# Kernel optimization log

Measured on AMD Instinct MI355X. Metric: run time of the kernel, lower is better.

Reference implementation:

```python
import jax, jax.numpy as jnp
import numpy as np
from jax import lax

THRESHOLDS = (0.25, 0.5, 0.75)
TAU = 100.0
NUM_CLASSES = 10
K = 32
RES_Z = 5.0
# each of the 16 binary logic gates is bilinear: g(a,b) = c0 + c1*a + c2*b + c3*a*b
GATE_COEF = jnp.array([
    [0, 0, 0, 0],   # 0: False
    [0, 0, 0, 1],   # 1: a AND b
    [0, 1, 0, -1],  # 2: a AND NOT b
    [0, 1, 0, 0],   # 3: a  (residual gate)
    [0, 0, 1, -1],  # 4: NOT a AND b
    [0, 0, 1, 0],   # 5: b
    [0, 1, 1, -2],  # 6: XOR
    [0, 1, 1, -1],  # 7: OR
    [1, -1, -1, 1], # 8: NOR
    [1, -1, -1, 2], # 9: XNOR
    [1, 0, -1, 0],  # 10: NOT b
    [1, 0, -1, 1],  # 11: a OR NOT b
    [1, -1, 0, 0],  # 12: NOT a
    [1, -1, 0, 1],  # 13: NOT a OR b
    [1, 0, 0, -1],  # 14: NAND
    [1, 0, 0, 0],   # 15: True
], dtype=jnp.float32)


def _gate_logits(key, shape):
    # residual init: pass-through gate (id 3) dominates
    w = 0.01 * jax.random.normal(key, shape, dtype=jnp.float32)
    return w.at[..., 3].add(RES_Z)


def _leaf_idx(rng, C, O, leaves=8, cpt=2, kk=9):
    # each tree uses cpt random input channels; each leaf picks one of them and a 3x3 position
    ch2 = rng.integers(0, C, size=(O, cpt))
    sel = rng.integers(0, cpt, size=(O, leaves))
    ch = np.take_along_axis(ch2, sel, axis=1)
    pos = rng.integers(0, kk, size=(O, leaves))
    return jnp.asarray(ch * kk + pos, dtype=jnp.int32)


def setup_inputs() -> dict:
    key = jax.random.key(0)
    ks = jax.random.split(key, 9)
    rng = np.random.default_rng(0)
    B = 128
    d = {"x": jax.random.uniform(ks[0], (B, 3, 32, 32), dtype=jnp.float32)}
    in_chs = [3 * len(THRESHOLDS), K, 4 * K, 16 * K]
    out_chs = [K, 4 * K, 16 * K, 32 * K]
    for i, (ci, co) in enumerate(zip(in_chs, out_chs)):
        d[f"c{i+1}_idx"] = _leaf_idx(rng, ci, co)
        d[f"c{i+1}_w"] = _gate_logits(ks[1 + i], (co, 7, 16))
    dims = [32 * K * 4, 1280 * K, 640 * K, 320 * K]
    for i in range(3):
        di, do = dims[i], dims[i + 1]
        d[f"l{i+1}_a"] = jnp.asarray(rng.integers(0, di, size=(do,)), dtype=jnp.int32)
        d[f"l{i+1}_b"] = jnp.asarray(rng.integers(0, di, size=(do,)), dtype=jnp.int32)
        d[f"l{i+1}_w"] = _gate_logits(ks[5 + i], (do, 16))
    return d


def _mix(logits):
    # softmax over 16 gates folded into 4 bilinear coefficients (fused gate mixture)
    return jax.nn.softmax(logits, axis=-1) @ GATE_COEF


def binarize(x):
    return jnp.concatenate([(x > t).astype(x.dtype) for t in THRESHOLDS], axis=1)


def tree_conv(x, leaf_idx, logits):
    # x: (B,C,H,W); leaf_idx: (O,8) into C*9 channel-major patch; logits: (O,7,16)
    B, C, H, W = x.shape
    xp = jnp.pad(x, ((0, 0), (0, 0), (1, 1), (1, 1)))
    patches = jnp.stack([xp[:, :, i:i + H, j:j + W] for i in range(3) for j in range(3)], axis=2)
    patches = patches.reshape(B, C * 9, H, W)
    vals = patches[:, leaf_idx]  # (B,O,8,H,W)
    m = _mix(logits)             # (O,7,4)
    node = 0
    for lvl in (4, 2, 1):
        a, b = vals[:, :, 0::2], vals[:, :, 1::2]
        w = m[:, node:node + lvl]  # (O,lvl,4)
        w0 = w[..., 0][None, :, :, None, None]
        w1 = w[..., 1][None, :, :, None, None]
        w2 = w[..., 2][None, :, :, None, None]
        w3 = w[..., 3][None, :, :, None, None]
        vals = w0 + w1 * a + w2 * b + w3 * (a * b)
        node += lvl
    return vals[:, :, 0]  # (B,O,H,W)


def or_pool(x):
    # OR of relaxed binary values == max pool 2x2/2
    return lax.reduce_window(x, -jnp.inf, lax.max, (1, 1, 2, 2), (1, 1, 2, 2), "VALID")


def logic_layer(x, a_idx, b_idx, logits):
    a = x[:, a_idx]  # (B,O)
    b = x[:, b_idx]
    w = _mix(logits)  # (O,4)
    return w[:, 0] + w[:, 1] * a + w[:, 2] * b + w[:, 3] * (a * b)


def group_sum(x):
    B = x.shape[0]
    return x.reshape(B, NUM_CLASSES, -1).sum(axis=-1) / TAU


def reference(x, c1_idx, c1_w, c2_idx, c2_w, c3_idx, c3_w, c4_idx, c4_w,
              l1_a, l1_b, l1_w, l2_a, l2_b, l2_w, l3_a, l3_b, l3_w):
    h = binarize(x)
    h = or_pool(tree_conv(h, c1_idx, c1_w))
    h = or_pool(tree_conv(h, c2_idx, c2_w))
    h = or_pool(tree_conv(h, c3_idx, c3_w))
    h = or_pool(tree_conv(h, c4_idx, c4_w))
    h = h.reshape(h.shape[0], -1)  # (B, 4096)
    h = logic_layer(h, l1_a, l1_b, l1_w)
    h = logic_layer(h, l2_a, l2_b, l2_w)
    h = logic_layer(h, l3_a, l3_b, l3_w)
    return group_sum(h)  # (B, 10)
```

## Files before the change

kernel.cpp:

```cpp
#include <hip/hip_runtime.h>
#include <hip/hip_fp16.h>

typedef float v2f __attribute__((ext_vector_type(2)));
typedef float v4f __attribute__((ext_vector_type(4)));
typedef int   v4i __attribute__((ext_vector_type(4)));

__device__ __constant__ float GC[16][4] = {
  {0,0,0,0},{0,0,0,1},{0,1,0,-1},{0,1,0,0},
  {0,0,1,-1},{0,0,1,0},{0,1,1,-2},{0,1,1,-1},
  {1,-1,-1,1},{1,-1,-1,2},{1,0,-1,0},{1,0,-1,1},
  {1,-1,0,0},{1,-1,0,1},{1,0,0,-1},{1,0,0,0}};

__device__ __forceinline__ v2f pk_mul(v2f a, v2f b) {
  v2f d;
  asm("v_pk_mul_f32 %0, %1, %2" : "=v"(d) : "v"(a), "v"(b));
  return d;
}
__device__ __forceinline__ v2f gate2pk(v2f a, v2f b, v2f w01, v2f w23) {
  v2f t = pk_mul(a, b);
  v2f d;
  asm("v_pk_fma_f32 %0, %1, %2, %2 op_sel:[0,1,0] op_sel_hi:[1,1,0]"
      : "=v"(d) : "v"(a), "v"(w01));
  asm("v_pk_fma_f32 %0, %1, %2, %0 op_sel:[0,0,0] op_sel_hi:[1,0,1]"
      : "+v"(d) : "v"(b), "v"(w23));
  asm("v_pk_fma_f32 %0, %1, %2, %0 op_sel:[0,1,0] op_sel_hi:[1,1,1]"
      : "+v"(d) : "v"(t), "v"(w23));
  return d;
}

__device__ __forceinline__ void mix_one(const float* lp, float* op) {
  float e[16];
  float s = 0.f;
  #pragma unroll
  for (int i = 0; i < 16; ++i) { e[i] = __expf(lp[i]); s += e[i]; }
  float inv = 1.0f / s;
  float w0 = 0.f, w1 = 0.f, w2 = 0.f, w3 = 0.f;
  #pragma unroll
  for (int i = 0; i < 16; ++i) {
    float p = e[i] * inv;
    w0 = fmaf(p, GC[i][0], w0);
    w1 = fmaf(p, GC[i][1], w1);
    w2 = fmaf(p, GC[i][2], w2);
    w3 = fmaf(p, GC[i][3], w3);
  }
  op[0] = w0; op[1] = w1; op[2] = w2; op[3] = w3;
}

struct PrepArgs {
  const float* logits[7];
  float* outm[7];
  const int* cidx[4];
  int* offt[4];
};

__global__ __launch_bounds__(256) void prep_k(PrepArgs A) {
  int gid = blockIdx.x * 256 + threadIdx.x;
  if (gid < 83552) {
    const int n[7] = {224, 896, 3584, 7168, 40960, 20480, 10240};
    int g = gid, seg = 0;
    while (seg < 6 && g >= n[seg]) { g -= n[seg]; ++seg; }
    mix_one(A.logits[seg] + (size_t)g * 16, A.outm[seg] + (size_t)g * 4);
  } else if (gid < 85248) {
    int r = gid - 83552;
    int L, rr;
    if (r < 32)       { L = 0; rr = r;       }
    else if (r < 160) { L = 1; rr = r - 32;  }
    else if (r < 672) { L = 2; rr = r - 160; }
    else              { L = 3; rr = r - 672; }
    const int W2Pt[4] = {35, 19, 12, 6};
    const int CSt[4]  = {1190, 342, 120, 37};
    const int swzt[4] = {1, 1, 1, 0};
    int W2P = W2Pt[L], CS = CSt[L], swz = swzt[L];
    const int* ci = A.cidx[L] + rr * 8;
    int* oo = A.offt[L] + rr * 8;
    #pragma unroll
    for (int l = 0; l < 8; ++l) {
      int idx = ci[l];
      int c  = idx / 9;
      int k  = idx - 9 * c;
      int di = k / 3 - 1;
      int dj = k - 3 * (k / 3) - 1;
      int yl = 1 + di;
      int off = c * CS + yl * W2P + 1 + dj;
      if (swz)
        off |= (((yl >> 1) & 1) << 28) | ((((yl + 1) >> 1) & 1) << 29);
      oo[l] = off;
    }
  }
}

struct MegaArgs {
  const float* x;
  const float* mc[4];
  const int*   offt[4];
  const int*   la[3];
  const int*   lb[3];
  const float* mlw[3];
  float* out;
};

extern __shared__ char S[];

template<int OH, int OW, int LOGOW, int IW2P, int PIXCNT, int LOGPIX,
         int NCH, int ITERS, bool UNI, bool RSWZ, bool OHALO, int OW2P,
         int OCS, bool OSWZ>
__device__ __forceinline__ void conv_stage(
    const float* in, float* outb,
    const int* __restrict__ offt, const float* __restrict__ mtab, int tid) {
  int pix = tid & (PIXCNT - 1);
  int ch0 = tid >> LOGPIX;
  int pw  = pix & (OW - 1);
  int ph  = pix >> LOGOW;
  int pixbase = 2 * ph * IW2P + 2 * pw;
  int ph1 = ph & 1;
  #pragma unroll 4
  for (int it = 0; it < ITERS; ++it) {
    int ch = ch0 + NCH * it;
    if (UNI) ch = __builtin_amdgcn_readfirstlane(ch);
    const int* ot = offt + ch * 8;
    const float* mt = mtab + ch * 28;
    v4f g0 = *(const v4f*)(mt +  0);
    v4f g1 = *(const v4f*)(mt +  4);
    v4f g2 = *(const v4f*)(mt +  8);
    v4f g3 = *(const v4f*)(mt + 12);
    v4f g4 = *(const v4f*)(mt + 16);
    v4f g5 = *(const v4f*)(mt + 20);
    v4f g6 = *(const v4f*)(mt + 24);
    v2f v01[8], v23[8];
    #pragma unroll
    for (int l = 0; l < 8; ++l) {
      int e = ot[l];
      int at, ab;
      if (RSWZ) {
        int off = e & 0x0FFFFFFF;
        at = off + pixbase + ((ph1 ^ (e >> 28)) & 1);
        ab = off + pixbase + IW2P + ((ph1 ^ (e >> 29)) & 1);
      } else {
        at = e + pixbase;
        ab = at + IW2P;
      }
      v2f t0; t0.x = in[at]; t0.y = in[at + 1];
      v2f t1; t1.x = in[ab]; t1.y = in[ab + 1];
      v01[l] = t0; v23[l] = t1;
    }
    v2f u0 = gate2pk(v01[0], v01[1], g0.xy, g0.zw);
    v2f u1 = gate2pk(v01[2], v01[3], g1.xy, g1.zw);
    v2f u2 = gate2pk(v01[4], v01[5], g2.xy, g2.zw);
    v2f u3 = gate2pk(v01[6], v01[7], g3.xy, g3.zw);
    v2f s0 = gate2pk(u0, u1, g4.xy, g4.zw);
    v2f s1 = gate2pk(u2, u3, g5.xy, g5.zw);
    v2f r0 = gate2pk(s0, s1, g6.xy, g6.zw);
    u0 = gate2pk(v23[0], v23[1], g0.xy, g0.zw);
    u1 = gate2pk(v23[2], v23[3], g1.xy, g1.zw);
    u2 = gate2pk(v23[4], v23[5], g2.xy, g2.zw);
    u3 = gate2pk(v23[6], v23[7], g3.xy, g3.zw);
    s0 = gate2pk(u0, u1, g4.xy, g4.zw);
    s1 = gate2pk(u2, u3, g5.xy, g5.zw);
    v2f r1 = gate2pk(s0, s1, g6.xy, g6.zw);
    float res = fmaxf(fmaxf(r0.x, r0.y), fmaxf(r1.x, r1.y));
    if (OHALO) {
      int oy = 1 + ph;
      int widx = ch * OCS + oy * OW2P + 1 + pw;
      if (OSWZ) widx += (oy >> 1) & 1;
      outb[widx] = res;
    } else {
      outb[ch * (OH * OW) + pix] = res;
    }
  }
}

__global__ __launch_bounds__(1024) void mega_k(MegaArgs A) {
  int tid = threadIdx.x;
  int b = blockIdx.x;
  float* binb = (float*)(S);
  float* buf1 = (float*)(S + 61440);
  float* buf2 = (float*)(S);
  float* buf3 = (float*)(S + 61440);
  float* h4   = (float*)(S);
  __half* g1h = (__half*)(S + 16384);
  __half* g2h = (__half*)(S + 98304);
  float* lsum = (float*)(S + 139264);
  const v4f z4 = {0.f, 0.f, 0.f, 0.f};

  for (int i = 4 * tid; i < 10712; i += 4096) *(v4f*)(binb + i) = z4;
  if (tid < 10) lsum[tid] = 0.f;
  __syncthreads();
  const float* xb = A.x + (size_t)b * 3072;
  #pragma unroll
  for (int i = 0; i < 3; ++i) {
    int idx = tid + 1024 * i;
    float v = xb[idx];
    int rgb = idx >> 10;
    int rem = idx & 1023;
    int y = rem >> 5, xx = rem & 31;
    int oy = 1 + y;
    int base = oy * 35 + 1 + xx + ((oy >> 1) & 1);
    binb[(0 + rgb) * 1190 + base] = v > 0.25f ? 1.f : 0.f;
    binb[(3 + rgb) * 1190 + base] = v > 0.50f ? 1.f : 0.f;
    binb[(6 + rgb) * 1190 + base] = v > 0.75f ? 1.f : 0.f;
  }
  __syncthreads();

  for (int i = 4 * tid; i < 10944; i += 4096) *(v4f*)(buf1 + i) = z4;
  __syncthreads();
  conv_stage<16,16,4, 35, 256,8, 4, 8, true, true, true, 19, 342, true>(
      binb, buf1, A.offt[0], A.mc[0], tid);
  __syncthreads();
  for (int i = 4 * tid; i < 15360; i += 4096) *(v4f*)(buf2 + i) = z4;
  __syncthreads();
  conv_stage<8,8,3, 19, 64,6, 16, 8, true, true, true, 12, 120, true>(
      buf1, buf2, A.offt[1], A.mc[1], tid);
  __syncthreads();
  for (int i = 4 * tid; i < 18944; i += 4096) *(v4f*)(buf3 + i) = z4;
  __syncthreads();
  conv_stage<4,4,2, 12, 16,4, 64, 8, false, true, true, 6, 37, false>(
      buf2, buf3, A.offt[2], A.mc[2], tid);
  __syncthreads();
  conv_stage<2,2,1, 6, 4,2, 256, 4, false, false, false, 1, 4, false>(
      buf3, h4, A.offt[3], A.mc[3], tid);
  __syncthreads();

  {
    const v4i* a4 = (const v4i*)A.la[0];
    const v4i* b4 = (const v4i*)A.lb[0];
    const v4f* w4 = (const v4f*)A.mlw[0];
    #pragma unroll 2
    for (int g = 0; g < 10; ++g) {
      int q = tid + 1024 * g;
      v4i ai = a4[q], bi = b4[q];
      float r[4];
      #pragma unroll
      for (int i = 0; i < 4; ++i) {
        v4f w = w4[4 * q + i];
        float a = h4[ai[i]], bb = h4[bi[i]];
        r[i] = fmaf(w.w, a * bb, fmaf(w.z, bb, fmaf(w.y, a, w.x)));
      }
      union { __half2 h[2]; uint2 u; } P;
      P.h[0] = __floats2half2_rn(r[0], r[1]);
      P.h[1] = __floats2half2_rn(r[2], r[3]);
      *(uint2*)(g1h + 4 * q) = P.u;
    }
  }
  __syncthreads();
  {
    const v4i* a4 = (const v4i*)A.la[1];
    const v4i* b4 = (const v4i*)A.lb[1];
    const v4f* w4 = (const v4f*)A.mlw[1];
    #pragma unroll 2
    for (int g = 0; g < 5; ++g) {
      int q = tid + 1024 * g;
      v4i ai = a4[q], bi = b4[q];
      float r[4];
      #pragma unroll
      for (int i = 0; i < 4; ++i) {
        v4f w = w4[4 * q + i];
        float a = __half2float(g1h[ai[i]]), bb = __half2float(g1h[bi[i]]);
        r[i] = fmaf(w.w, a * bb, fmaf(w.z, bb, fmaf(w.y, a, w.x)));
      }
      union { __half2 h[2]; uint2 u; } P;
      P.h[0] = __floats2half2_rn(r[0], r[1]);
      P.h[1] = __floats2half2_rn(r[2], r[3]);
      *(uint2*)(g2h + 4 * q) = P.u;
    }
  }
  __syncthreads();
  {
    const v4i* a4 = (const v4i*)A.la[2];
    const v4i* b4 = (const v4i*)A.lb[2];
    const v4f* w4 = (const v4f*)A.mlw[2];
    int lane = tid & 63;
    #pragma unroll
    for (int g = 0; g < 3; ++g) {
      int q = tid + 1024 * g;
      if (q < 2560) {
        v4i ai = a4[q], bi = b4[q];
        float s = 0.f;
        #pragma unroll
        for (int i = 0; i < 4; ++i) {
          v4f w = w4[4 * q + i];
          float a = __half2float(g2h[ai[i]]), bb = __half2float(g2h[bi[i]]);
          s += fmaf(w.w, a * bb, fmaf(w.z, bb, fmaf(w.y, a, w.x)));
        }
        #pragma unroll
        for (int m = 1; m < 64; m <<= 1) s += __shfl_xor(s, m);
        if (lane == 0) atomicAdd(&lsum[q >> 8], s);
      }
    }
  }
  __syncthreads();
  if (tid < 10) A.out[b * 10 + tid] = lsum[tid] * 0.01f;
}

extern "C" void kernel_launch(void* const* d_in, const int* in_sizes, int n_in,
                              void* d_out, int out_size, void* d_ws, size_t ws_size,
                              hipStream_t stream) {
  const float* x   = (const float*)d_in[0];
  const int*   c1i = (const int*)d_in[1];
  const float* c1w = (const float*)d_in[2];
  const int*   c2i = (const int*)d_in[3];
  const float* c2w = (const float*)d_in[4];
  const int*   c3i = (const int*)d_in[5];
  const float* c3w = (const float*)d_in[6];
  const int*   c4i = (const int*)d_in[7];
  const float* c4w = (const float*)d_in[8];
  const int*   l1a = (const int*)d_in[9];
  const int*   l1b = (const int*)d_in[10];
  const float* l1w = (const float*)d_in[11];
  const int*   l2a = (const int*)d_in[12];
  const int*   l2b = (const int*)d_in[13];
  const float* l2w = (const float*)d_in[14];
  const int*   l3a = (const int*)d_in[15];
  const int*   l3b = (const int*)d_in[16];
  const float* l3w = (const float*)d_in[17];

  float* ws = (float*)d_ws;
  float* mc1 = ws;
  float* mc2 = mc1 + 896;
  float* mc3 = mc2 + 3584;
  float* mc4 = mc3 + 14336;
  float* ml1 = mc4 + 28672;
  float* ml2 = ml1 + 163840;
  float* ml3 = ml2 + 81920;
  int* off1 = (int*)(ml3 + 40960);
  int* off2 = off1 + 256;
  int* off3 = off2 + 1024;
  int* off4 = off3 + 4096;

  PrepArgs P;
  P.logits[0] = c1w; P.outm[0] = mc1;
  P.logits[1] = c2w; P.outm[1] = mc2;
  P.logits[2] = c3w; P.outm[2] = mc3;
  P.logits[3] = c4w; P.outm[3] = mc4;
  P.logits[4] = l1w; P.outm[4] = ml1;
  P.logits[5] = l2w; P.outm[5] = ml2;
  P.logits[6] = l3w; P.outm[6] = ml3;
  P.cidx[0] = c1i; P.offt[0] = off1;
  P.cidx[1] = c2i; P.offt[1] = off2;
  P.cidx[2] = c3i; P.offt[2] = off3;
  P.cidx[3] = c4i; P.offt[3] = off4;
  prep_k<<<333, 256, 0, stream>>>(P);

  MegaArgs M;
  M.x = x;
  M.mc[0] = mc1; M.mc[1] = mc2; M.mc[2] = mc3; M.mc[3] = mc4;
  M.offt[0] = off1; M.offt[1] = off2; M.offt[2] = off3; M.offt[3] = off4;
  M.la[0] = l1a; M.lb[0] = l1b; M.mlw[0] = ml1;
  M.la[1] = l2a; M.lb[1] = l2b; M.mlw[1] = ml2;
  M.la[2] = l3a; M.lb[2] = l3b; M.mlw[2] = ml3;
  M.out = (float*)d_out;

  static bool attr_set = false;
  if (!attr_set) {
    hipFuncSetAttribute((const void*)mega_k,
                        hipFuncAttributeMaxDynamicSharedMemorySize, 139328);
    attr_set = true;
  }
  mega_k<<<128, 1024, 139328, stream>>>(M);
}
```

Baseline: 155.5 us.

## Split each sample across two blocks with global-memory halo exchange

Launches two blocks per sample instead of one, each computing half the rows of every conv stage and half the outputs of every logic layer. After each stage the blocks exchange boundary rows or layer halves through a global workspace, synchronised by per-sample atomic flags with release/acquire spin-waits. The aim is to use 256 CUs on the MI355X rather than 128. The cost is extra global traffic, many cross-block barriers, and a deadlock risk if the two blocks of a pair are not co-resident, since both must be running at the same time for the spin-waits to complete.

```diff
diff --git a/kernel.cpp b/kernel.cpp
--- a/kernel.cpp
+++ b/kernel.cpp
@@ -51,6 +51,7 @@
   float* outm[7];
   const int* cidx[4];
   int* offt[4];
+  int* flags;
 };
 
 __global__ __launch_bounds__(256) void prep_k(PrepArgs A) {
@@ -68,7 +69,7 @@
     else if (r < 672) { L = 2; rr = r - 160; }
     else              { L = 3; rr = r - 672; }
     const int W2Pt[4] = {35, 19, 12, 6};
-    const int CSt[4]  = {1190, 342, 120, 37};
+    const int CSt[4]  = {1190, 342, 121, 37};
     const int swzt[4] = {1, 1, 1, 0};
     int W2P = W2Pt[L], CS = CSt[L], swz = swzt[L];
     const int* ci = A.cidx[L] + rr * 8;
@@ -86,6 +87,8 @@
         off |= (((yl >> 1) & 1) << 28) | ((((yl + 1) >> 1) & 1) << 29);
       oo[l] = off;
     }
+  } else if (gid < 86272) {
+    A.flags[gid - 85248] = 0;
   }
 }
 
@@ -96,21 +99,24 @@
   const int*   la[3];
   const int*   lb[3];
   const float* mlw[3];
+  int*   flags;
+  float* ex;
   float* out;
 };
 
 extern __shared__ char S[];
 
-template<int OH, int OW, int LOGOW, int IW2P, int PIXCNT, int LOGPIX,
+template<int OWF, int LOGOW, int IW2P, int PIXH, int LOGPIXH,
          int NCH, int ITERS, bool UNI, bool RSWZ, bool OHALO, int OW2P,
-         int OCS, bool OSWZ>
+         int OCS, bool OSWZ, int OHW>
 __device__ __forceinline__ void conv_stage(
     const float* in, float* outb,
-    const int* __restrict__ offt, const float* __restrict__ mtab, int tid) {
-  int pix = tid & (PIXCNT - 1);
-  int ch0 = tid >> LOGPIX;
-  int pw  = pix & (OW - 1);
-  int ph  = pix >> LOGOW;
+    const int* __restrict__ offt, const float* __restrict__ mtab,
+    int tid, int ph0) {
+  int pix = tid & (PIXH - 1);
+  int ch0 = tid >> LOGPIXH;
+  int pw  = pix & (OWF - 1);
+  int ph  = (pix >> LOGOW) + ph0;
   int pixbase = 2 * ph * IW2P + 2 * pw;
   int ph1 = ph & 1;
   #pragma unroll 4
@@ -164,23 +170,44 @@
       if (OSWZ) widx += (oy >> 1) & 1;
       outb[widx] = res;
     } else {
-      outb[ch * (OH * OW) + pix] = res;
-    }
-  }
+      outb[ch * OHW + ph * OWF + pw] = res;
+    }
+  }
+}
+
+__device__ __forceinline__ void sigf(int* f) {
+  if (threadIdx.x == 0)
+    __hip_atomic_fetch_add(f, 1, __ATOMIC_RELEASE, __HIP_MEMORY_SCOPE_AGENT);
+}
+__device__ __forceinline__ void waitf(int* f, int v) {
+  if (threadIdx.x == 0)
+    while (__hip_atomic_load(f, __ATOMIC_ACQUIRE, __HIP_MEMORY_SCOPE_AGENT) < v)
+      __builtin_amdgcn_s_sleep(8);
 }
 
 __global__ __launch_bounds__(1024) void mega_k(MegaArgs A) {
   int tid = threadIdx.x;
-  int b = blockIdx.x;
+  int b = blockIdx.x & 127;
+  int h = blockIdx.x >> 7;
+  int hp = 1 - h;
   float* binb = (float*)(S);
-  float* buf1 = (float*)(S + 61440);
+  float* buf1 = (float*)(S + 61952);
   float* buf2 = (float*)(S);
-  float* buf3 = (float*)(S + 61440);
+  float* buf3 = (float*)(S + 61952);
   float* h4   = (float*)(S);
   __half* g1h = (__half*)(S + 16384);
   __half* g2h = (__half*)(S + 98304);
   float* lsum = (float*)(S + 139264);
   const v4f z4 = {0.f, 0.f, 0.f, 0.f};
+
+  int*   flg = A.flags + b * 8;
+  float* exb = A.ex + (size_t)b * 46080;
+  float* e1g  = exb;
+  float* e2g  = exb + 1216;
+  float* e3g  = exb + 4288;
+  float* e4g  = exb + 10432;
+  float* eg1g = exb + 14528;
+  float* eg2g = exb + 35008;
 
   for (int i = 4 * tid; i < 10712; i += 4096) *(v4f*)(binb + i) = z4;
   if (tid < 10) lsum[tid] = 0.f;
@@ -203,21 +230,82 @@
 
   for (int i = 4 * tid; i < 10944; i += 4096) *(v4f*)(buf1 + i) = z4;
   __syncthreads();
-  conv_stage<16,16,4, 35, 256,8, 4, 8, true, true, true, 19, 342, true>(
-      binb, buf1, A.offt[0], A.mc[0], tid);
-  __syncthreads();
-  for (int i = 4 * tid; i < 15360; i += 4096) *(v4f*)(buf2 + i) = z4;
-  __syncthreads();
-  conv_stage<8,8,3, 19, 64,6, 16, 8, true, true, true, 12, 120, true>(
-      buf1, buf2, A.offt[1], A.mc[1], tid);
+  conv_stage<16,4,35,128,7, 8,4, true, true, true,19,342,true, 256>(
+      binb, buf1, A.offt[0], A.mc[0], tid, 8 * h);
+  __syncthreads();
+  for (int i = 4 * tid; i < 15488; i += 4096) *(v4f*)(buf2 + i) = z4;
+  if (tid < 608) {
+    int c = tid / 19, x = tid - c * 19;
+    e1g[h * 608 + tid] = buf1[c * 342 + (8 + h) * 19 + x];
+  }
+  __threadfence();
+  __syncthreads();
+  sigf(flg + 0);
+  waitf(flg + 0, 2);
+  __syncthreads();
+  if (tid < 608) {
+    int c = tid / 19, x = tid - c * 19;
+    buf1[c * 342 + (9 - h) * 19 + x] = e1g[hp * 608 + tid];
+  }
+  __syncthreads();
+
+  conv_stage<8,3,19,32,5, 32,4, false, true, true,12,121,true, 64>(
+      buf1, buf2, A.offt[1], A.mc[1], tid, 4 * h);
   __syncthreads();
   for (int i = 4 * tid; i < 18944; i += 4096) *(v4f*)(buf3 + i) = z4;
-  __syncthreads();
-  conv_stage<4,4,2, 12, 16,4, 64, 8, false, true, true, 6, 37, false>(
-      buf2, buf3, A.offt[2], A.mc[2], tid);
-  __syncthreads();
-  conv_stage<2,2,1, 6, 4,2, 256, 4, false, false, false, 1, 4, false>(
-      buf3, h4, A.offt[3], A.mc[3], tid);
+  for (int i = tid; i < 1536; i += 1024) {
+    int c = i / 12, x = i - c * 12;
+    e2g[h * 1536 + i] = buf2[c * 121 + (4 + h) * 12 + x];
+  }
+  __threadfence();
+  __syncthreads();
+  sigf(flg + 1);
+  waitf(flg + 1, 2);
+  __syncthreads();
+  for (int i = tid; i < 1536; i += 1024) {
+    int c = i / 12, x = i - c * 12;
+    buf2[c * 121 + (5 - h) * 12 + x] = e2g[hp * 1536 + i];
+  }
+  __syncthreads();
+
+  conv_stage<4,2,12,8,3, 128,4, false, true, true,6,37,false, 16>(
+      buf2, buf3, A.offt[2], A.mc[2], tid, 2 * h);
+  __syncthreads();
+  for (int i = tid; i < 3072; i += 1024) {
+    int c = i / 6, x = i - c * 6;
+    e3g[h * 3072 + i] = buf3[c * 37 + (2 + h) * 6 + x];
+  }
+  __threadfence();
+  __syncthreads();
+  sigf(flg + 2);
+  waitf(flg + 2, 2);
+  __syncthreads();
+  for (int i = tid; i < 3072; i += 1024) {
+    int c = i / 6, x = i - c * 6;
+    buf3[c * 37 + (3 - h) * 6 + x] = e3g[hp * 3072 + i];
+  }
+  __syncthreads();
+
+  conv_stage<2,1,6,2,1, 512,2, false, false, false,1,4,false, 4>(
+      buf3, h4, A.offt[3], A.mc[3], tid, h);
+  __syncthreads();
+  #pragma unroll
+  for (int g = 0; g < 2; ++g) {
+    int t2 = tid + 1024 * g;
+    int c = t2 >> 1, j = t2 & 1;
+    e4g[h * 2048 + t2] = h4[c * 4 + 2 * h + j];
+  }
+  __threadfence();
+  __syncthreads();
+  sigf(flg + 3);
+  waitf(flg + 3, 2);
+  __syncthreads();
+  #pragma unroll
+  for (int g = 0; g < 2; ++g) {
+    int t2 = tid + 1024 * g;
+    int c = t2 >> 1, j = t2 & 1;
+    h4[c * 4 + 2 * hp + j] = e4g[hp * 2048 + t2];
+  }
   __syncthreads();
 
   {
@@ -225,8 +313,8 @@
     const v4i* b4 = (const v4i*)A.lb[0];
     const v4f* w4 = (const v4f*)A.mlw[0];
     #pragma unroll 2
-    for (int g = 0; g < 10; ++g) {
-      int q = tid + 1024 * g;
+    for (int g = 0; g < 5; ++g) {
+      int q = h * 5120 + tid + 1024 * g;
       v4i ai = a4[q], bi = b4[q];
       float r[4];
       #pragma unroll
@@ -235,44 +323,76 @@
         float a = h4[ai[i]], bb = h4[bi[i]];
         r[i] = fmaf(w.w, a * bb, fmaf(w.z, bb, fmaf(w.y, a, w.x)));
       }
-      union { __half2 h[2]; uint2 u; } P;
-      P.h[0] = __floats2half2_rn(r[0], r[1]);
-      P.h[1] = __floats2half2_rn(r[2], r[3]);
+      union { __half2 hh[2]; uint2 u; } P;
+      P.hh[0] = __floats2half2_rn(r[0], r[1]);
+      P.hh[1] = __floats2half2_rn(r[2], r[3]);
       *(uint2*)(g1h + 4 * q) = P.u;
     }
   }
   __syncthreads();
+  {
+    float* g1f = (float*)g1h;
+    #pragma unroll
+    for (int g = 0; g < 10; ++g) { int i = tid + 1024 * g; eg1g[h * 10240 + i] = g1f[h * 10240 + i]; }
+    __threadfence();
+    __syncthreads();
+    sigf(flg + 4);
+    waitf(flg + 4, 2);
+    __syncthreads();
+    #pragma unroll
+    for (int g = 0; g < 10; ++g) { int i = tid + 1024 * g; g1f[hp * 10240 + i] = eg1g[hp * 10240 + i]; }
+  }
+  __syncthreads();
+
   {
     const v4i* a4 = (const v4i*)A.la[1];
     const v4i* b4 = (const v4i*)A.lb[1];
     const v4f* w4 = (const v4f*)A.mlw[1];
     #pragma unroll 2
-    for (int g = 0; g < 5; ++g) {
-      int q = tid + 1024 * g;
-      v4i ai = a4[q], bi = b4[q];
-      float r[4];
-      #pragma unroll
-      for (int i = 0; i < 4; ++i) {
-        v4f w = w4[4 * q + i];
-        float a = __half2float(g1h[ai[i]]), bb = __half2float(g1h[bi[i]]);
-        r[i] = fmaf(w.w, a * bb, fmaf(w.z, bb, fmaf(w.y, a, w.x)));
+    for (int g = 0; g < 3; ++g) {
+      int qr = tid + 1024 * g;
+      if (qr < 2560) {
+        int q = h * 2560 + qr;
+        v4i ai = a4[q], bi = b4[q];
+        float r[4];
+        #pragma unroll
+        for (int i = 0; i < 4; ++i) {
+          v4f w = w4[4 * q + i];
+          float a = __half2float(g1h[ai[i]]), bb = __half2float(g1h[bi[i]]);
+          r[i] = fmaf(w.w, a * bb, fmaf(w.z, bb, fmaf(w.y, a, w.x)));
+        }
+        union { __half2 hh[2]; uint2 u; } P;
+        P.hh[0] = __floats2half2_rn(r[0], r[1]);
+        P.hh[1] = __floats2half2_rn(r[2], r[3]);
+        *(uint2*)(g2h + 4 * q) = P.u;
       }
-      union { __half2 h[2]; uint2 u; } P;
-      P.h[0] = __floats2half2_rn(r[0], r[1]);
-      P.h[1] = __floats2half2_rn(r[2], r[3]);
-      *(uint2*)(g2h + 4 * q) = P.u;
-    }
-  }
-  __syncthreads();
+    }
+  }
+  __syncthreads();
+  {
+    float* g2f = (float*)g2h;
+    #pragma unroll
+    for (int g = 0; g < 5; ++g) { int i = tid + 1024 * g; eg2g[h * 5120 + i] = g2f[h * 5120 + i]; }
+    __threadfence();
+    __syncthreads();
+    sigf(flg + 5);
+    waitf(flg + 5, 2);
+    __syncthreads();
+    #pragma unroll
+    for (int g = 0; g < 5; ++g) { int i = tid + 1024 * g; g2f[hp * 5120 + i] = eg2g[hp * 5120 + i]; }
+  }
+  __syncthreads();
+
   {
     const v4i* a4 = (const v4i*)A.la[2];
     const v4i* b4 = (const v4i*)A.lb[2];
     const v4f* w4 = (const v4f*)A.mlw[2];
     int lane = tid & 63;
     #pragma unroll
-    for (int g = 0; g < 3; ++g) {
-      int q = tid + 1024 * g;
-      if (q < 2560) {
+    for (int g = 0; g < 2; ++g) {
+      int qr = tid + 1024 * g;
+      if (qr < 1280) {
+        int q = h * 1280 + qr;
         v4i ai = a4[q], bi = b4[q];
         float s = 0.f;
         #pragma unroll
@@ -288,7 +408,7 @@
     }
   }
   __syncthreads();
-  if (tid < 10) A.out[b * 10 + tid] = lsum[tid] * 0.01f;
+  if (tid < 5) A.out[b * 10 + 5 * h + tid] = lsum[5 * h + tid] * 0.01f;
 }
 
 extern "C" void kernel_launch(void* const* d_in, const int* in_sizes, int n_in,
@@ -325,6 +445,8 @@
   int* off2 = off1 + 256;
   int* off3 = off2 + 1024;
   int* off4 = off3 + 4096;
+  int* flags = off4 + 8192;
+  float* ex = (float*)(flags + 1024);
 
   PrepArgs P;
   P.logits[0] = c1w; P.outm[0] = mc1;
@@ -338,7 +460,8 @@
   P.cidx[1] = c2i; P.offt[1] = off2;
   P.cidx[2] = c3i; P.offt[2] = off3;
   P.cidx[3] = c4i; P.offt[3] = off4;
-  prep_k<<<333, 256, 0, stream>>>(P);
+  P.flags = flags;
+  prep_k<<<337, 256, 0, stream>>>(P);
 
   MegaArgs M;
   M.x = x;
@@ -347,6 +470,8 @@
   M.la[0] = l1a; M.lb[0] = l1b; M.mlw[0] = ml1;
   M.la[1] = l2a; M.lb[1] = l2b; M.mlw[1] = ml2;
   M.la[2] = l3a; M.lb[2] = l3b; M.mlw[2] = ml3;
+  M.flags = flags;
+  M.ex = ex;
   M.out = (float*)d_out;
 
   static bool attr_set = false;
@@ -355,5 +480,5 @@
                         hipFuncAttributeMaxDynamicSharedMemorySize, 139328);
     attr_set = true;
   }
-  mega_k<<<128, 1024, 139328, stream>>>(M);
-}
+  mega_k<<<256, 1024, 139328, stream>>>(M);
+}
```

Measured after the change: 598.1 us. 3.85x slower.

## Store conv activations as duplicated half pairs to fetch each pixel pair in one LDS load

Applied to the files above, without the earlier changes.

Conv-stage intermediate buffers are switched from fp32 to fp16. Each value is written twice into adjacent halves, so a single 32-bit __half2 load returns the horizontal pixel pair, halving LDS load instructions per leaf. Buffer offsets and a channel stride are adjusted to keep alignment. The cost is fp16 rounding of intermediate activations, extra half writes, and conversion instructions on read.

```diff
diff --git a/kernel.cpp b/kernel.cpp
--- a/kernel.cpp
+++ b/kernel.cpp
@@ -26,6 +26,11 @@
   asm("v_pk_fma_f32 %0, %1, %2, %0 op_sel:[0,1,0] op_sel_hi:[1,1,1]"
       : "+v"(d) : "v"(t), "v"(w23));
   return d;
+}
+
+__device__ __forceinline__ v2f h2f(__half2 h) {
+  float2 f = __half22float2(h);
+  return v2f{f.x, f.y};
 }
 
 __device__ __forceinline__ void mix_one(const float* lp, float* op) {
@@ -68,7 +73,7 @@
     else if (r < 672) { L = 2; rr = r - 160; }
     else              { L = 3; rr = r - 672; }
     const int W2Pt[4] = {35, 19, 12, 6};
-    const int CSt[4]  = {1190, 342, 120, 37};
+    const int CSt[4]  = {1190, 342, 121, 37};
     const int swzt[4] = {1, 1, 1, 0};
     int W2P = W2Pt[L], CS = CSt[L], swz = swzt[L];
     const int* ci = A.cidx[L] + rr * 8;
@@ -103,9 +108,9 @@
 
 template<int OH, int OW, int LOGOW, int IW2P, int PIXCNT, int LOGPIX,
          int NCH, int ITERS, bool UNI, bool RSWZ, bool OHALO, int OW2P,
-         int OCS, bool OSWZ>
+         int OCS, bool OSWZ, bool FOUT>
 __device__ __forceinline__ void conv_stage(
-    const float* in, float* outb,
+    const __half2* in, void* outb,
     const int* __restrict__ offt, const float* __restrict__ mtab, int tid) {
   int pix = tid & (PIXCNT - 1);
   int ch0 = tid >> LOGPIX;
@@ -139,9 +144,8 @@
         at = e + pixbase;
         ab = at + IW2P;
       }
-      v2f t0; t0.x = in[at]; t0.y = in[at + 1];
-      v2f t1; t1.x = in[ab]; t1.y = in[ab + 1];
-      v01[l] = t0; v23[l] = t1;
+      v01[l] = h2f(in[at]);
+      v23[l] = h2f(in[ab]);
     }
     v2f u0 = gate2pk(v01[0], v01[1], g0.xy, g0.zw);
     v2f u1 = gate2pk(v01[2], v01[3], g1.xy, g1.zw);
@@ -162,9 +166,12 @@
       int oy = 1 + ph;
       int widx = ch * OCS + oy * OW2P + 1 + pw;
       if (OSWZ) widx += (oy >> 1) & 1;
-      outb[widx] = res;
-    } else {
-      outb[ch * (OH * OW) + pix] = res;
+      __half hv = __float2half(res);
+      __half* ob = (__half*)outb;
+      ob[2 * widx] = hv;
+      ob[2 * widx - 1] = hv;
+    } else if (FOUT) {
+      ((float*)outb)[ch * (OH * OW) + pix] = res;
     }
   }
 }
@@ -172,20 +179,21 @@
 __global__ __launch_bounds__(1024) void mega_k(MegaArgs A) {
   int tid = threadIdx.x;
   int b = blockIdx.x;
-  float* binb = (float*)(S);
-  float* buf1 = (float*)(S + 61440);
-  float* buf2 = (float*)(S);
-  float* buf3 = (float*)(S + 61440);
+  __half2* binb = (__half2*)(S);
+  __half2* buf1 = (__half2*)(S + 61952);
+  __half2* buf2 = (__half2*)(S);
+  __half2* buf3 = (__half2*)(S + 61952);
   float* h4   = (float*)(S);
   __half* g1h = (__half*)(S + 16384);
   __half* g2h = (__half*)(S + 98304);
   float* lsum = (float*)(S + 139264);
   const v4f z4 = {0.f, 0.f, 0.f, 0.f};
 
-  for (int i = 4 * tid; i < 10712; i += 4096) *(v4f*)(binb + i) = z4;
+  for (int i = 4 * tid; i < 10712; i += 4096) *(v4f*)((float*)binb + i) = z4;
   if (tid < 10) lsum[tid] = 0.f;
   __syncthreads();
   const float* xb = A.x + (size_t)b * 3072;
+  __half* binh = (__half*)binb;
   #pragma unroll
   for (int i = 0; i < 3; ++i) {
     int idx = tid + 1024 * i;
@@ -195,28 +203,33 @@
     int y = rem >> 5, xx = rem & 31;
     int oy = 1 + y;
     int base = oy * 35 + 1 + xx + ((oy >> 1) & 1);
-    binb[(0 + rgb) * 1190 + base] = v > 0.25f ? 1.f : 0.f;
-    binb[(3 + rgb) * 1190 + base] = v > 0.50f ? 1.f : 0.f;
-    binb[(6 + rgb) * 1190 + base] = v > 0.75f ? 1.f : 0.f;
-  }
-  __syncthreads();
-
-  for (int i = 4 * tid; i < 10944; i += 4096) *(v4f*)(buf1 + i) = z4;
-  __syncthreads();
-  conv_stage<16,16,4, 35, 256,8, 4, 8, true, true, true, 19, 342, true>(
+    #pragma unroll
+    for (int t = 0; t < 3; ++t) {
+      float th = 0.25f * (float)(t + 1);
+      __half hv = __float2half(v > th ? 1.f : 0.f);
+      int e = (3 * t + rgb) * 1190 + base;
+      binh[2 * e] = hv;
+      binh[2 * e - 1] = hv;
+    }
+  }
+  __syncthreads();
+
+  for (int i = 4 * tid; i < 10944; i += 4096) *(v4f*)((float*)buf1 + i) = z4;
+  __syncthreads();
+  conv_stage<16,16,4, 35, 256,8, 4, 8, true, true, true, 19, 342, true, false>(
       binb, buf1, A.offt[0], A.mc[0], tid);
   __syncthreads();
-  for (int i = 4 * tid; i < 15360; i += 4096) *(v4f*)(buf2 + i) = z4;
-  __syncthreads();
-  conv_stage<8,8,3, 19, 64,6, 16, 8, true, true, true, 12, 120, true>(
+  for (int i = 4 * tid; i < 15488; i += 4096) *(v4f*)((float*)buf2 + i) = z4;
+  __syncthreads();
+  conv_stage<8,8,3, 19, 64,6, 16, 8, true, true, true, 12, 121, true, false>(
       buf1, buf2, A.offt[1], A.mc[1], tid);
   __syncthreads();
-  for (int i = 4 * tid; i < 18944; i += 4096) *(v4f*)(buf3 + i) = z4;
-  __syncthreads();
-  conv_stage<4,4,2, 12, 16,4, 64, 8, false, true, true, 6, 37, false>(
+  for (int i = 4 * tid; i < 18944; i += 4096) *(v4f*)((float*)buf3 + i) = z4;
+  __syncthreads();
+  conv_stage<4,4,2, 12, 16,4, 64, 8, false, true, true, 6, 37, false, false>(
       buf2, buf3, A.offt[2], A.mc[2], tid);
   __syncthreads();
-  conv_stage<2,2,1, 6, 4,2, 256, 4, false, false, false, 1, 4, false>(
+  conv_stage<2,2,1, 6, 4,2, 256, 4, false, false, false, 1, 4, false, true>(
       buf3, h4, A.offt[3], A.mc[3], tid);
   __syncthreads();
 
@@ -235,9 +248,9 @@
         float a = h4[ai[i]], bb = h4[bi[i]];
         r[i] = fmaf(w.w, a * bb, fmaf(w.z, bb, fmaf(w.y, a, w.x)));
       }
-      union { __half2 h[2]; uint2 u; } P;
-      P.h[0] = __floats2half2_rn(r[0], r[1]);
-      P.h[1] = __floats2half2_rn(r[2], r[3]);
+      union { __half2 hh[2]; uint2 u; } P;
+      P.hh[0] = __floats2half2_rn(r[0], r[1]);
+      P.hh[1] = __floats2half2_rn(r[2], r[3]);
       *(uint2*)(g1h + 4 * q) = P.u;
     }
   }
@@ -257,9 +270,9 @@
         float a = __half2float(g1h[ai[i]]), bb = __half2float(g1h[bi[i]]);
         r[i] = fmaf(w.w, a * bb, fmaf(w.z, bb, fmaf(w.y, a, w.x)));
       }
-      union { __half2 h[2]; uint2 u; } P;
-      P.h[0] = __floats2half2_rn(r[0], r[1]);
-      P.h[1] = __floats2half2_rn(r[2], r[3]);
+      union { __half2 hh[2]; uint2 u; } P;
+      P.hh[0] = __floats2half2_rn(r[0], r[1]);
+      P.hh[1] = __floats2half2_rn(r[2], r[3]);
       *(uint2*)(g2h + 4 * q) = P.u;
     }
   }
```

Result: slower. 169.8 us (+9.2%).
